# Kernel optimization log

Measured on AMD Instinct MI355X. Metric: run time of the kernel, lower is better.

## Reference

```python
import jax, jax.numpy as jnp
import numpy as np

TAU = 1.0
LAM = 1.0


def _l2_normalize(x, axis=-1, eps=1e-12):
    n = jnp.sqrt(jnp.sum(x * x, axis=axis, keepdims=True))
    return x / jnp.maximum(n, eps)


def setup_inputs() -> dict:
    key = jax.random.key(0)
    k1, k2, k3, k4 = jax.random.split(key, 4)
    B, D = 4096, 512
    return {
        "mu": jax.random.normal(k1, (B, D), dtype=jnp.float32),
        "mu_cap": jax.random.normal(k2, (B, D), dtype=jnp.float32),
        "log_var": jax.random.normal(k3, (B, D), dtype=jnp.float32),
        "log_var_cap": jax.random.normal(k4, (B, D), dtype=jnp.float32),
    }


def _supcon(features, labels, tau):
    # features: [N, D], labels: [N]
    N = features.shape[0]
    Xn = _l2_normalize(features, axis=-1)
    sim = Xn @ Xn.T                                   # [N, N] cosine similarities
    eye = jnp.eye(N, dtype=bool)
    sim = jnp.where(eye, -jnp.inf, sim)               # fill_diagonal_(-inf)
    ls = jax.nn.log_softmax(sim / tau, axis=-1)
    ls = jnp.where(eye, 0.0, ls)                      # fill_diagonal_(0)
    mask = (labels[:, None] == labels[None, :]).astype(jnp.float32)
    mask = jnp.where(eye, 0.0, mask)
    num_pos = jnp.sum(mask, axis=-1)
    pos_avg = jnp.sum(ls * mask, axis=-1) / (num_pos + 1e-5)
    return -jnp.sum(pos_avg) / N


def _kl_div(mu1, mu2, logvar1, logvar2):
    var1 = jnp.exp(logvar1)
    var2 = jnp.exp(logvar2)
    part1 = (var1 + 1e-8) / (var2 + 1e-8)
    part2 = logvar2 - logvar1
    part3 = jnp.square(mu1 - mu2) / (var2 + 1e-8)
    return 0.5 * jnp.sum(part1 + part2 + part3 - 1.0, axis=1)


def reference(mu, mu_cap, log_var, log_var_cap):
    B, D = mu.shape
    # reparameterization (fixed noise for a deterministic reference)
    ek1, ek2 = jax.random.split(jax.random.key(42))
    eps1 = jax.random.normal(ek1, (B, D), dtype=mu.dtype)
    eps2 = jax.random.normal(ek2, (B, D), dtype=mu.dtype)
    x = mu + jnp.exp(0.5 * log_var) * eps1
    x_cap = mu_cap + jnp.exp(0.5 * log_var_cap) * eps2

    # SimCLR: concat views, fake labels [0..B-1, 0..B-1]
    feats = jnp.concatenate([x, x_cap], axis=0)       # [2B, D]
    labels = jnp.concatenate([jnp.arange(B), jnp.arange(B)])
    base_loss = _supcon(feats, labels, TAU)

    # distribution alignment (JSD between Gaussians), on L2-normalized stats
    mu_n = _l2_normalize(mu, axis=1)
    lv_n = _l2_normalize(log_var, axis=1)
    mu_cn = _l2_normalize(mu_cap, axis=1)
    lv_cn = _l2_normalize(log_var_cap, axis=1)
    mu_m = 0.5 * (mu_n + mu_cn)
    log_var_m = jnp.log(0.5 * (jnp.exp(lv_n) + jnp.exp(lv_cn)) + 1e-8)
    kl1 = _kl_div(mu_n, mu_m, lv_n, log_var_m)
    kl2 = _kl_div(mu_cn, mu_m, lv_cn, log_var_m)
    jsd = jnp.mean(0.5 * (kl1 + kl2))

    return base_loss + LAM * jsd
```

## Files before the change

### kernel.cpp

```cpp
#include <hip/hip_runtime.h>
#include <hip/hip_bf16.h>
#include <stdint.h>


typedef __attribute__((ext_vector_type(4))) float f32x4;
typedef __attribute__((ext_vector_type(8))) short bf16x8;

#define NSLOT 32
#define NGK   16

__device__ __forceinline__ void tf_round(uint32_t& x0, uint32_t& x1, int r){
  x0 += x1;
  x1 = (x1 << r) | (x1 >> (32 - r));
  x1 ^= x0;
}

__device__ __forceinline__ void threefry2x32(uint32_t k0, uint32_t k1,
                                             uint32_t c0, uint32_t c1,
                                             uint32_t& o0, uint32_t& o1){
  uint32_t ks2 = k0 ^ k1 ^ 0x1BD11BDAu;
  uint32_t x0 = c0 + k0, x1 = c1 + k1;
  tf_round(x0,x1,13); tf_round(x0,x1,15); tf_round(x0,x1,26); tf_round(x0,x1,6);
  x0 += k1; x1 += ks2 + 1u;
  tf_round(x0,x1,17); tf_round(x0,x1,29); tf_round(x0,x1,16); tf_round(x0,x1,24);
  x0 += ks2; x1 += k0 + 2u;
  tf_round(x0,x1,13); tf_round(x0,x1,15); tf_round(x0,x1,26); tf_round(x0,x1,6);
  x0 += k0; x1 += k1 + 3u;
  tf_round(x0,x1,17); tf_round(x0,x1,29); tf_round(x0,x1,16); tf_round(x0,x1,24);
  x0 += k1; x1 += ks2 + 4u;
  tf_round(x0,x1,13); tf_round(x0,x1,15); tf_round(x0,x1,26); tf_round(x0,x1,6);
  x0 += ks2; x1 += k0 + 5u;
  o0 = x0; o1 = x1;
}

__device__ __forceinline__ float erfinv_f32(float x){
  float w = -log1pf(-x*x);
  float p;
  if (w < 5.0f){
    w -= 2.5f;
    p = 2.81022636e-08f;
    p = fmaf(p,w, 3.43273939e-07f);
    p = fmaf(p,w,-3.5233877e-06f);
    p = fmaf(p,w,-4.39150654e-06f);
    p = fmaf(p,w, 0.00021858087f);
    p = fmaf(p,w,-0.00125372503f);
    p = fmaf(p,w,-0.00417768164f);
    p = fmaf(p,w, 0.246640727f);
    p = fmaf(p,w, 1.50140941f);
  } else {
    w = sqrtf(w) - 3.0f;
    p = -0.000200214257f;
    p = fmaf(p,w, 0.000100950558f);
    p = fmaf(p,w, 0.00134934322f);
    p = fmaf(p,w,-0.00367342844f);
    p = fmaf(p,w, 0.00573950773f);
    p = fmaf(p,w,-0.0076224613f);
    p = fmaf(p,w, 0.00943887047f);
    p = fmaf(p,w, 1.00167406f);
    p = fmaf(p,w, 2.83297682f);
  }
  return p*x;
}

__device__ __forceinline__ float bits2normal(uint32_t bits){
  float f = __uint_as_float((bits >> 9) | 0x3F800000u) - 1.0f;
  const float lo = -0.99999994f;
  float v = fmaf(f, 2.0f, lo);
  v = fmaxf(lo, v);
  return 1.41421354f * erfinv_f32(v);
}

__device__ __forceinline__ unsigned short f2bf(float f){
  uint32_t u = __float_as_uint(f);
  u += 0x7FFFu + ((u >> 16) & 1u);
  return (unsigned short)(u >> 16);
}

__global__ __launch_bounds__(256) void k_featsjsd(const float* __restrict__ mu,
                                                  const float* __restrict__ mu_cap,
                                                  const float* __restrict__ lv,
                                                  const float* __restrict__ lv_cap,
                                                  unsigned short* __restrict__ Xn,
                                                  float* __restrict__ jsd_row){
  int r = blockIdx.x;
  int t = threadIdx.x;

  uint32_t a0,a1,b0,b1;
  threefry2x32(0u, 42u, 0u, 2u, a0, b0);
  threefry2x32(0u, 42u, 1u, 3u, a1, b1);

  float m[2][2], mc[2][2], av[2][2], bv[2][2], x[2][2], xc[2][2];
  float s[2][6] = {{0,0,0,0,0,0},{0,0,0,0,0,0}};

  #pragma unroll
  for (int h = 0; h < 2; ++h){
    size_t base = (size_t)(r + h*2048) * 512;
    float2 m2  = *(const float2*)(mu     + base + 2*t);
    float2 mc2 = *(const float2*)(mu_cap + base + 2*t);
    float2 av2 = *(const float2*)(lv     + base + 2*t);
    float2 bv2 = *(const float2*)(lv_cap + base + 2*t);
    m[h][0]=m2.x;  m[h][1]=m2.y;  mc[h][0]=mc2.x; mc[h][1]=mc2.y;
    av[h][0]=av2.x; av[h][1]=av2.y; bv[h][0]=bv2.x; bv[h][1]=bv2.y;
  }

  #pragma unroll
  for (int q = 0; q < 2; ++q){
    uint32_t p = (uint32_t)r*512u + (uint32_t)(2*t + q);
    uint32_t oa0, oa1, ob0, ob1;
    threefry2x32(a0, a1, p, p + 0x100000u, oa0, oa1);
    threefry2x32(b0, b1, p, p + 0x100000u, ob0, ob1);
    float e1[2] = {bits2normal(oa0), bits2normal(oa1)};
    float e2[2] = {bits2normal(ob0), bits2normal(ob1)};
    #pragma unroll
    for (int h = 0; h < 2; ++h){
      x[h][q]  = m[h][q]  + __expf(0.5f*av[h][q]) * e1[h];
      xc[h][q] = mc[h][q] + __expf(0.5f*bv[h][q]) * e2[h];
      s[h][0] += x[h][q]*x[h][q];   s[h][1] += xc[h][q]*xc[h][q];
      s[h][2] += m[h][q]*m[h][q];   s[h][3] += mc[h][q]*mc[h][q];
      s[h][4] += av[h][q]*av[h][q]; s[h][5] += bv[h][q]*bv[h][q];
    }
  }

  __shared__ float sred[4][12];
  #pragma unroll
  for (int h = 0; h < 2; ++h)
    #pragma unroll
    for (int k = 0; k < 6; ++k){
      float v = s[h][k];
      #pragma unroll
      for (int o = 32; o; o >>= 1) v += __shfl_down(v, o);
      if ((t & 63) == 0) sred[t >> 6][h*6 + k] = v;
      s[h][k] = v;
    }
  __syncthreads();
  float tot[2][6];
  #pragma unroll
  for (int h = 0; h < 2; ++h)
    #pragma unroll
    for (int k = 0; k < 6; ++k)
      tot[h][k] = sred[0][h*6+k] + sred[1][h*6+k] + sred[2][h*6+k] + sred[3][h*6+k];

  float accv[2] = {0.f, 0.f};
  #pragma unroll
  for (int h = 0; h < 2; ++h){
    float ix  = 1.f / fmaxf(sqrtf(tot[h][0]), 1e-12f);
    float ixc = 1.f / fmaxf(sqrtf(tot[h][1]), 1e-12f);
    float im  = 1.f / fmaxf(sqrtf(tot[h][2]), 1e-12f);
    float imc = 1.f / fmaxf(sqrtf(tot[h][3]), 1e-12f);
    float ia  = 1.f / fmaxf(sqrtf(tot[h][4]), 1e-12f);
    float ib  = 1.f / fmaxf(sqrtf(tot[h][5]), 1e-12f);

    unsigned short xb[2], xcb[2];
    #pragma unroll
    for (int q = 0; q < 2; ++q){
      xb[q]  = f2bf(x[h][q]  * ix);
      xcb[q] = f2bf(xc[h][q] * ixc);
      float an = m[h][q]*im, bn = mc[h][q]*imc;
      float al = av[h][q]*ia, bl = bv[h][q]*ib;
      float ea = __expf(al), eb = __expf(bl);
      float varm = 0.5f*(ea + eb);
      float lvm  = __logf(varm + 1e-8f);
      float v2   = __expf(lvm);
      float den  = v2 + 1e-8f;
      float dm   = 0.5f*(an - bn);
      float dm2  = dm*dm;
      accv[h] += (ea + 1e-8f)/den + (lvm - al) + dm2/den - 1.f;
      accv[h] += (eb + 1e-8f)/den + (lvm - bl) + dm2/den - 1.f;
    }
    size_t base = (size_t)(r + h*2048) * 512;
    *(uint32_t*)&Xn[base + 2*t] = xb[0] | ((uint32_t)xb[1] << 16);
    *(uint32_t*)&Xn[(size_t)4096*512 + base + 2*t] = xcb[0] | ((uint32_t)xcb[1] << 16);
  }

  __shared__ float sred2[4][2];
  #pragma unroll
  for (int h = 0; h < 2; ++h){
    float v = accv[h];
    #pragma unroll
    for (int o = 32; o; o >>= 1) v += __shfl_down(v, o);
    if ((t & 63) == 0) sred2[t >> 6][h] = v;
  }
  __syncthreads();
  if (t < 2)
    jsd_row[r + t*2048] = 0.25f * (sred2[0][t]+sred2[1][t]+sred2[2][t]+sred2[3][t]);
}

__device__ __forceinline__ void gload_lds16(const unsigned short* g, unsigned short* l){
  __builtin_amdgcn_global_load_lds(
      (const __attribute__((address_space(1))) void*)g,
      (__attribute__((address_space(3))) void*)l, 16, 0, 0);
}

__device__ __forceinline__ void stage_slot(const unsigned short* __restrict__ Xn,
                                           unsigned short* S, int slot, int pbase,
                                           int gk, int wid, int prow, int pcol){
  const unsigned short* g = Xn + (size_t)(pbase + wid*32 + prow)*512 + gk*32 + pcol;
  gload_lds16(g,          &S[slot*8192 + (wid*2  )*512]);
  gload_lds16(g + 16*512, &S[slot*8192 + (wid*2+1)*512]);
}

__global__ __launch_bounds__(512, 1) void k_simlse(const unsigned short* __restrict__ Xn,
                                                   float* __restrict__ rowsumP,
                                                   float* __restrict__ possim){
  int bid = (blockIdx.x & 7)*64 + (blockIdx.x >> 3);

  __shared__ unsigned short SA[4*8192];
  __shared__ unsigned short SB[4*8192];
  __shared__ float redR[4][256];
  __shared__ float redC[2][256];

  int tid = threadIdx.x;
  int wid = tid >> 6, l = tid & 63;
  int wr = wid >> 2, wn = wid & 3;
  int l15 = l & 15, l4 = l >> 4;

  int prow = (l >> 3)*2 + (((l & 7) ^ (l >> 3)) >> 2);
  int pcol = (((l & 7) ^ (l >> 3)) & 3) * 8;

  const int idx8 = (((l15 & 1) << 2) | l4) ^ (l15 >> 1);
  const int aoff = wr*4096 + (l15 >> 1)*64 + idx8*8;
  const int boff = wn*2048 + (l15 >> 1)*64 + idx8*8;

  int ntile, rb0, cb0, rb1, cb1;
  if (bid < 16){
    ntile = 2;
    rb0 = cb0 = 2*bid;
    rb1 = cb1 = 2*bid + 1;
  } else {
    ntile = 1;
    int j = bid - 16, rbb = 0, rem = 31;
    while (j >= rem){ j -= rem; --rem; ++rbb; }
    rb0 = rbb; cb0 = rbb + 1 + j;
    rb1 = cb1 = 0;
  }

  for (int tile = 0; tile < ntile; ++tile){
    int rb = tile ? rb1 : rb0;
    int cb = tile ? cb1 : cb0;
    int rowbase = rb*256, colbase = cb*256;
    bool diag    = (rb == cb);
    bool postile = (cb == rb + 16);

    f32x4 acc[8][4];
    #pragma unroll
    for (int m = 0; m < 8; ++m)
      #pragma unroll
      for (int n = 0; n < 4; ++n) acc[m][n] = f32x4{0.f,0.f,0.f,0.f};

    if (tile) __syncthreads();

    #pragma unroll
    for (int g0 = 0; g0 < 3; ++g0){
      stage_slot(Xn, SA, g0, rowbase, g0, wid, prow, pcol);
      stage_slot(Xn, SB, g0, colbase, g0, wid, prow, pcol);
      __builtin_amdgcn_sched_barrier(0);
    }

    for (int gk = 0; gk < NGK; ++gk){
      const unsigned short* SAb = &SA[(gk & 3)*8192];
      const unsigned short* SBb = &SB[(gk & 3)*8192];
      int sgk = gk + 3;
      int ss  = sgk & 3;

      if (gk <= NGK-3)      asm volatile("s_waitcnt vmcnt(8)" ::: "memory");
      else if (gk == NGK-2) asm volatile("s_waitcnt vmcnt(4)" ::: "memory");
      else                  asm volatile("s_waitcnt vmcnt(0)" ::: "memory");
      __builtin_amdgcn_s_barrier();

      bf16x8 bfr[4], af[4];
      #pragma unroll
      for (int n = 0; n < 4; ++n)
        bfr[n] = *(const bf16x8*)&SBb[boff + n*512];
      #pragma unroll
      for (int mi = 0; mi < 4; ++mi)
        af[mi] = *(const bf16x8*)&SAb[aoff + mi*512];
      if (sgk < NGK) stage_slot(Xn, SA, ss, rowbase, sgk, wid, prow, pcol);
      asm volatile("s_waitcnt lgkmcnt(0)" ::: "memory");
      __builtin_amdgcn_sched_barrier(0);
      __builtin_amdgcn_s_setprio(1);
      #pragma unroll
      for (int mi = 0; mi < 4; ++mi)
        #pragma unroll
        for (int n = 0; n < 4; ++n)
          acc[mi][n] = __builtin_amdgcn_mfma_f32_16x16x32_bf16(af[mi], bfr[n], acc[mi][n], 0, 0, 0);
      __builtin_amdgcn_s_setprio(0);
      __builtin_amdgcn_s_barrier();

      #pragma unroll
      for (int mi = 0; mi < 4; ++mi)
        af[mi] = *(const bf16x8*)&SAb[aoff + 2048 + mi*512];
      if (sgk < NGK) stage_slot(Xn, SB, ss, colbase, sgk, wid, prow, pcol);
      asm volatile("s_waitcnt lgkmcnt(0)" ::: "memory");
      __builtin_amdgcn_sched_barrier(0);
      __builtin_amdgcn_s_setprio(1);
      #pragma unroll
      for (int mi = 0; mi < 4; ++mi)
        #pragma unroll
        for (int n = 0; n < 4; ++n)
          acc[4+mi][n] = __builtin_amdgcn_mfma_f32_16x16x32_bf16(af[mi], bfr[n], acc[4+mi][n], 0, 0, 0);
      __builtin_amdgcn_s_setprio(0);
      __builtin_amdgcn_s_barrier();
    }

    #pragma unroll
    for (int m = 0; m < 8; ++m){
      #pragma unroll
      for (int n = 0; n < 4; ++n){
        int col_l = wn*64 + n*16 + l15;
        #pragma unroll
        for (int r = 0; r < 4; ++r){
          int row_l = wr*128 + m*16 + l4*4 + r;
          float v = acc[m][n][r];
          if (postile && row_l == col_l){
            possim[rowbase + row_l] = v;
            possim[colbase + col_l] = v;
          }
          float e = __expf(v);
          if (diag && row_l == col_l) e = 0.f;
          acc[m][n][r] = e;
        }
      }
    }

    #pragma unroll
    for (int m = 0; m < 8; ++m){
      #pragma unroll
      for (int r = 0; r < 4; ++r){
        float s = acc[m][0][r] + acc[m][1][r] + acc[m][2][r] + acc[m][3][r];
        s += __shfl_xor(s, 1); s += __shfl_xor(s, 2);
        s += __shfl_xor(s, 4); s += __shfl_xor(s, 8);
        if (l15 == 0) redR[wn][wr*128 + m*16 + l4*4 + r] = s;
      }
    }
    #pragma unroll
    for (int n = 0; n < 4; ++n){
      float s = 0.f;
      #pragma unroll
      for (int m = 0; m < 8; ++m)
        #pragma unroll
        for (int r = 0; r < 4; ++r) s += acc[m][n][r];
      s += __shfl_xor(s, 16); s += __shfl_xor(s, 32);
      if (l4 == 0) redC[wr][wn*64 + n*16 + l15] = s;
    }
    __syncthreads();
    if (tid < 256){
      float rs = redR[0][tid] + redR[1][tid] + redR[2][tid] + redR[3][tid];
      rowsumP[(size_t)cb*8192 + rowbase + tid] = rs;
      if (!diag){
        float cs = redC[0][tid] + redC[1][tid];
        rowsumP[(size_t)rb*8192 + colbase + tid] = cs;
      }
    }
  }
}

__global__ __launch_bounds__(256) void k_lsepart(const float* __restrict__ rowsumP,
                                                 const float* __restrict__ possim,
                                                 float* __restrict__ part){
  int t = threadIdx.x;
  int row = blockIdx.x*64 + (t & 63);
  int g = t >> 6;
  float s = 0.f;
  #pragma unroll
  for (int cs = 0; cs < 8; ++cs)
    s += rowsumP[(size_t)(g*8 + cs)*8192 + row];
  __shared__ float partial[4][64];
  partial[g][t & 63] = s;
  __syncthreads();
  if (t < 64){
    float tot = partial[0][t] + partial[1][t] + partial[2][t] + partial[3][t];
    float v = __logf(tot) - possim[row];
    #pragma unroll
    for (int o = 32; o; o >>= 1) v += __shfl_down(v, o);
    if (t == 0) part[blockIdx.x] = v;
  }
}

__global__ __launch_bounds__(256) void k_final(const float* __restrict__ part,
                                               const float* __restrict__ jsd_row,
                                               float* __restrict__ out){
  int t = threadIdx.x;
  float s = (t < 128) ? part[t] : 0.f;
  float j = 0.f;
  #pragma unroll
  for (int q = 0; q < 16; ++q) j += jsd_row[t + q*256];

  __shared__ float sr[4], jr[4];
  float ss = s, jj = j;
  #pragma unroll
  for (int o = 32; o; o >>= 1){ ss += __shfl_down(ss, o); jj += __shfl_down(jj, o); }
  if ((t & 63) == 0){ sr[t >> 6] = ss; jr[t >> 6] = jj; }
  __syncthreads();
  if (t == 0){
    float base = (sr[0]+sr[1]+sr[2]+sr[3]) / (8192.f * (1.f + 1e-5f));
    float jsd  = (jr[0]+jr[1]+jr[2]+jr[3]) / 4096.f;
    out[0] = base + jsd;
  }
}

extern "C" void kernel_launch(void* const* d_in, const int* in_sizes, int n_in,
                              void* d_out, int out_size, void* d_ws, size_t ws_size,
                              hipStream_t stream) {
  const float* mu     = (const float*)d_in[0];
  const float* mu_cap = (const float*)d_in[1];
  const float* lv     = (const float*)d_in[2];
  const float* lv_cap = (const float*)d_in[3];
  float* out = (float*)d_out;

  char* w = (char*)d_ws;
  unsigned short* Xn = (unsigned short*)w;
  float* rowsumP = (float*)(w + 8388608);
  float* possim  = (float*)(w + 8388608 + 1048576);
  float* jsd_row = (float*)(w + 8388608 + 1048576 + 32768);
  float* part    = (float*)(w + 8388608 + 1048576 + 32768 + 16384);

  k_featsjsd<<<2048, 256, 0, stream>>>(mu, mu_cap, lv, lv_cap, Xn, jsd_row);
  k_simlse  <<<512,  512, 0, stream>>>(Xn, rowsumP, possim);
  k_lsepart <<<128,  256, 0, stream>>>(rowsumP, possim, part);
  k_final   <<<1,    256, 0, stream>>>(part, jsd_row, out);
}
```

Measured before the change: 101.9 us.

## Software-pipeline LDS fragment loads across K-steps with register double buffering

Restructures the main GEMM K-loop so the next step's A/B fragments are read from LDS while the current MFMAs run, using ping-pong register buffers and partial lgkmcnt waits instead of full drains. The loop is unrolled by two to swap the buffers statically, and the vmcnt thresholds are retuned to match. Launch bounds also change to request two blocks per CU, which lowers the register budget while the kernel now holds extra fragment registers. This may cause spills, and the LDS footprint may not allow two blocks anyway.

```diff
diff --git a/kernel.cpp b/kernel.cpp
--- a/kernel.cpp
+++ b/kernel.cpp
@@ -130,7 +130,6 @@
       #pragma unroll
       for (int o = 32; o; o >>= 1) v += __shfl_down(v, o);
       if ((t & 63) == 0) sred[t >> 6][h*6 + k] = v;
-      s[h][k] = v;
     }
   __syncthreads();
   float tot[2][6];
@@ -199,7 +198,63 @@
   gload_lds16(g + 16*512, &S[slot*8192 + (wid*2+1)*512]);
 }
 
-__global__ __launch_bounds__(512, 1) void k_simlse(const unsigned short* __restrict__ Xn,
+__device__ __forceinline__ void gk_body(
+    int gk, const unsigned short* __restrict__ Xn,
+    unsigned short* SA, unsigned short* SB,
+    int rowbase, int colbase, int wid, int prow, int pcol,
+    int aoff, int boff,
+    bf16x8 (&af0c)[4], bf16x8 (&bfc)[4],
+    bf16x8 (&af0n)[4], bf16x8 (&bfn)[4],
+    bf16x8 (&af1)[4],
+    f32x4 (&acc)[8][4])
+{
+  const unsigned short* SAb = &SA[(gk & 3)*8192];
+
+  #pragma unroll
+  for (int mi = 0; mi < 4; ++mi)
+    af1[mi] = *(const bf16x8*)&SAb[aoff + 2048 + mi*512];
+  if (gk + 3 < NGK)
+    stage_slot(Xn, SA, (gk+3)&3, rowbase, gk+3, wid, prow, pcol);
+  asm volatile("s_waitcnt lgkmcnt(4)" ::: "memory");
+  __builtin_amdgcn_sched_barrier(0);
+  __builtin_amdgcn_s_setprio(1);
+  #pragma unroll
+  for (int mi = 0; mi < 4; ++mi)
+    #pragma unroll
+    for (int n = 0; n < 4; ++n)
+      acc[mi][n] = __builtin_amdgcn_mfma_f32_16x16x32_bf16(af0c[mi], bfc[n], acc[mi][n], 0, 0, 0);
+  __builtin_amdgcn_s_setprio(0);
+  if (gk <= 12)      asm volatile("s_waitcnt vmcnt(6)" ::: "memory");
+  else if (gk == 13) asm volatile("s_waitcnt vmcnt(4)" ::: "memory");
+  else if (gk == 14) asm volatile("s_waitcnt vmcnt(0)" ::: "memory");
+  __builtin_amdgcn_s_barrier();
+
+  if (gk + 1 < NGK){
+    const unsigned short* SAn = &SA[((gk+1) & 3)*8192];
+    const unsigned short* SBn = &SB[((gk+1) & 3)*8192];
+    #pragma unroll
+    for (int n = 0; n < 4; ++n)
+      bfn[n] = *(const bf16x8*)&SBn[boff + n*512];
+    #pragma unroll
+    for (int mi = 0; mi < 4; ++mi)
+      af0n[mi] = *(const bf16x8*)&SAn[aoff + mi*512];
+  }
+  if (gk + 3 < NGK)
+    stage_slot(Xn, SB, (gk+3)&3, colbase, gk+3, wid, prow, pcol);
+  if (gk + 1 < NGK) asm volatile("s_waitcnt lgkmcnt(8)" ::: "memory");
+  else              asm volatile("s_waitcnt lgkmcnt(0)" ::: "memory");
+  __builtin_amdgcn_sched_barrier(0);
+  __builtin_amdgcn_s_setprio(1);
+  #pragma unroll
+  for (int mi = 0; mi < 4; ++mi)
+    #pragma unroll
+    for (int n = 0; n < 4; ++n)
+      acc[4+mi][n] = __builtin_amdgcn_mfma_f32_16x16x32_bf16(af1[mi], bfc[n], acc[4+mi][n], 0, 0, 0);
+  __builtin_amdgcn_s_setprio(0);
+  __builtin_amdgcn_s_barrier();
+}
+
+__global__ __launch_bounds__(512, 2) void k_simlse(const unsigned short* __restrict__ Xn,
                                                    float* __restrict__ rowsumP,
                                                    float* __restrict__ possim){
   int bid = (blockIdx.x & 7)*64 + (blockIdx.x >> 3);
@@ -234,6 +289,8 @@
     rb1 = cb1 = 0;
   }
 
+  bf16x8 af0a[4], af0b[4], bfa[4], bfb[4], af1[4];
+
   for (int tile = 0; tile < ntile; ++tile){
     int rb = tile ? rb1 : rb0;
     int cb = tile ? cb1 : cb0;
@@ -253,53 +310,23 @@
     for (int g0 = 0; g0 < 3; ++g0){
       stage_slot(Xn, SA, g0, rowbase, g0, wid, prow, pcol);
       stage_slot(Xn, SB, g0, colbase, g0, wid, prow, pcol);
-      __builtin_amdgcn_sched_barrier(0);
-    }
-
-    for (int gk = 0; gk < NGK; ++gk){
-      const unsigned short* SAb = &SA[(gk & 3)*8192];
-      const unsigned short* SBb = &SB[(gk & 3)*8192];
-      int sgk = gk + 3;
-      int ss  = sgk & 3;
-
-      if (gk <= NGK-3)      asm volatile("s_waitcnt vmcnt(8)" ::: "memory");
-      else if (gk == NGK-2) asm volatile("s_waitcnt vmcnt(4)" ::: "memory");
-      else                  asm volatile("s_waitcnt vmcnt(0)" ::: "memory");
-      __builtin_amdgcn_s_barrier();
-
-      bf16x8 bfr[4], af[4];
-      #pragma unroll
-      for (int n = 0; n < 4; ++n)
-        bfr[n] = *(const bf16x8*)&SBb[boff + n*512];
-      #pragma unroll
-      for (int mi = 0; mi < 4; ++mi)
-        af[mi] = *(const bf16x8*)&SAb[aoff + mi*512];
-      if (sgk < NGK) stage_slot(Xn, SA, ss, rowbase, sgk, wid, prow, pcol);
-      asm volatile("s_waitcnt lgkmcnt(0)" ::: "memory");
-      __builtin_amdgcn_sched_barrier(0);
-      __builtin_amdgcn_s_setprio(1);
-      #pragma unroll
-      for (int mi = 0; mi < 4; ++mi)
-        #pragma unroll
-        for (int n = 0; n < 4; ++n)
-          acc[mi][n] = __builtin_amdgcn_mfma_f32_16x16x32_bf16(af[mi], bfr[n], acc[mi][n], 0, 0, 0);
-      __builtin_amdgcn_s_setprio(0);
-      __builtin_amdgcn_s_barrier();
-
-      #pragma unroll
-      for (int mi = 0; mi < 4; ++mi)
-        af[mi] = *(const bf16x8*)&SAb[aoff + 2048 + mi*512];
-      if (sgk < NGK) stage_slot(Xn, SB, ss, colbase, sgk, wid, prow, pcol);
-      asm volatile("s_waitcnt lgkmcnt(0)" ::: "memory");
-      __builtin_amdgcn_sched_barrier(0);
-      __builtin_amdgcn_s_setprio(1);
-      #pragma unroll
-      for (int mi = 0; mi < 4; ++mi)
-        #pragma unroll
-        for (int n = 0; n < 4; ++n)
-          acc[4+mi][n] = __builtin_amdgcn_mfma_f32_16x16x32_bf16(af[mi], bfr[n], acc[4+mi][n], 0, 0, 0);
-      __builtin_amdgcn_s_setprio(0);
-      __builtin_amdgcn_s_barrier();
+    }
+    asm volatile("s_waitcnt vmcnt(8)" ::: "memory");
+    __builtin_amdgcn_s_barrier();
+
+    #pragma unroll
+    for (int n = 0; n < 4; ++n)
+      bfa[n] = *(const bf16x8*)&SB[boff + n*512];
+    #pragma unroll
+    for (int mi = 0; mi < 4; ++mi)
+      af0a[mi] = *(const bf16x8*)&SA[aoff + mi*512];
+
+    #pragma unroll
+    for (int gk = 0; gk < NGK; gk += 2){
+      gk_body(gk,   Xn, SA, SB, rowbase, colbase, wid, prow, pcol, aoff, boff,
+              af0a, bfa, af0b, bfb, af1, acc);
+      gk_body(gk+1, Xn, SA, SB, rowbase, colbase, wid, prow, pcol, aoff, boff,
+              af0b, bfb, af0a, bfa, af1, acc);
     }
 
     #pragma unroll
```

Result: no change. 103.3 us (+1.4%).
